# Performance work log

Measured on AMD Instinct MI355X. Metric: run time of the kernel, lower is better.

The kernel has to match this reference:

```python
import jax, jax.numpy as jnp
from jax import lax
import numpy as np

# correlation hyperparams (from init_kwargs)
MAX_D = 32      # maxDisplacement
PAD = 1         # zero padding
K = 3           # patch (kernel) size
STRIDE_K = 1    # stride over output pixels
STRIDE_D = 1    # stride over displacements


def setup_inputs() -> dict:
    key = jax.random.key(0)
    k0, k1 = jax.random.split(key)
    x0 = jax.random.normal(k0, (4, 64, 256, 512), dtype=jnp.float32)
    x1 = jax.random.normal(k1, (4, 64, 256, 512), dtype=jnp.float32)
    return {"x0": x0, "x1": x1}


def _corr2d(x0, x1):
    # x0, x1: [B, C, H, W] NCHW feature maps
    B, C, H, W = x0.shape
    # zero-pad spatially; x1 gets extra width padding so all displacements are in-bounds
    x0p = jnp.pad(x0, ((0, 0), (0, 0), (PAD, PAD), (PAD, PAD)))
    x1p = jnp.pad(x1, ((0, 0), (0, 0), (PAD, PAD), (PAD + MAX_D, PAD + MAX_D)))
    Wp = W + 2 * PAD
    # width offsets into x1p for displacements d = -MAX_D .. MAX_D step STRIDE_D
    offsets = jnp.arange(0, 2 * MAX_D + 1, STRIDE_D, dtype=jnp.int32)

    def step(carry, off):
        x1s = lax.dynamic_slice_in_dim(x1p, off, Wp, axis=3)   # [B,C,Hp,Wp]
        prod = jnp.sum(x0p * x1s, axis=1)                      # channel dot -> [B,Hp,Wp]
        # KxK box-sum over the patch, stride STRIDE_K -> [B,Ho,Wo]
        s = lax.reduce_window(prod, jnp.float32(0), lax.add,
                              (1, K, K), (1, STRIDE_K, STRIDE_K), 'VALID')
        return carry, s

    _, out = lax.scan(step, None, offsets)        # [nD, B, Ho, Wo]
    out = jnp.transpose(out, (1, 0, 2, 3))        # [B, nD, Ho, Wo]
    return out / jnp.asarray(K * K * C, out.dtype)


def reference(x0, x1):
    return _corr2d(x0, x1)
```

## Files before the change

kernel.cpp:

```cpp
#include <hip/hip_runtime.h>

#define WF 512
#define HF 256
#define CF 64
#define NDTOT 65
#define DP 72

static constexpr size_t CH  = (size_t)HF * WF;
static constexpr size_t WH  = (size_t)HF * WF;
static constexpr float  INV = 1.0f / 576.0f;

typedef _Float16 f16;
typedef _Float16 f16x4 __attribute__((ext_vector_type(4)));
typedef _Float16 f16x8 __attribute__((ext_vector_type(8)));
typedef float    f32x4 __attribute__((ext_vector_type(4)));

#if __has_builtin(__builtin_amdgcn_mfma_f32_16x16x16f16)
#define MFMA16(A, B, C) __builtin_amdgcn_mfma_f32_16x16x16f16((A), (B), (C), 0, 0, 0)
#define FRAG_T f16x4
__device__ __forceinline__ f16x4 mkfrag(f16 a, f16 b, f16 c, f16 d) {
    f16x4 r; r[0] = a; r[1] = b; r[2] = c; r[3] = d; return r;
}
#else
#define MFMA16(A, B, C) __builtin_amdgcn_mfma_f32_16x16x32_f16((A), (B), (C), 0, 0, 0)
#define FRAG_T f16x8
__device__ __forceinline__ f16x8 mkfrag(f16 a, f16 b, f16 c, f16 d) {
    f16x8 r; r[0] = a; r[1] = b; r[2] = c; r[3] = d;
    r[4] = (f16)0.f; r[5] = (f16)0.f; r[6] = (f16)0.f; r[7] = (f16)0.f; return r;
}
#endif

#define GLOADF(dst, ptr, offbytes) \
    asm volatile("global_load_dword %0, %1, %2" \
                 : "=v"(dst) : "v"(offbytes), "s"(ptr))

__global__ __launch_bounds__(256) __attribute__((amdgpu_waves_per_eu(2, 4)))
void corr_gram(const float* __restrict__ x0, const float* __restrict__ x1,
               f16* __restrict__ ws) {
    const int f = blockIdx.x;
    const int tid = (f & 7) * 512 + (f >> 3);
    const int b = tid >> 10;
    const int y = (tid >> 2) & 255;
    const int sg = tid & 3;

    const int t = threadIdx.x;
    const int l = t & 63;
    const int w = t >> 6;
    const int xs = (sg * 4 + w) * 32;
    const int jb = xs - 32;

    const int n  = l & 15;
    const int kq = l >> 4;
    const int sn = (n & 3) ^ (n >> 2);

    __shared__ float lds[8192];
    float* base = lds + w * 2048;

    const float* x0r = x0 + (size_t)b * CF * CH + (size_t)y * WF;
    const float* x1r = x1 + (size_t)b * CF * CH + (size_t)y * WF;

    const int c0 = l & 31, qa = l >> 5;
    const int sA = (c0 & 3) ^ ((c0 >> 2) & 3);
    int aoff[2], awad[2];
    aoff[0] = (4 * qa) * (int)CH + xs + c0;
    aoff[1] = (4 * (qa + 2)) * (int)CH + xs + c0;
    awad[0] = c0 * 16 + 4 * (qa ^ sA);
    awad[1] = c0 * 16 + 4 * ((qa + 2) ^ sA);
    int boff[6], bwad[6];
#pragma unroll
    for (int u = 0; u < 6; ++u) {
        const int v = u * 64 + l;
        const int q = v / 96;
        const int cb = v - 96 * q;
        int jg = jb + cb;
        jg = jg < 0 ? 0 : (jg > 511 ? 511 : jg);
        boff[u] = (4 * q) * (int)CH + jg;
        bwad[u] = 512 + cb * 16 + 4 * (q ^ ((cb & 3) ^ ((cb >> 2) & 3)));
    }

    int ard[2], brd[6];
#pragma unroll
    for (int xt = 0; xt < 2; ++xt) ard[xt] = (16 * xt + n) * 16 + 4 * (kq ^ sn);
#pragma unroll
    for (int jt = 0; jt < 6; ++jt) brd[jt] = 512 + (16 * jt + n) * 16 + 4 * (kq ^ sn);
    bool okj[6];
#pragma unroll
    for (int jt = 0; jt < 6; ++jt) okj[jt] = (unsigned)(jb + 16 * jt + n) < (unsigned)WF;

    f32x4 acc[10];
#pragma unroll
    for (int i = 0; i < 10; ++i) acc[i] = (f32x4)0.0f;

    float ra[8], rb[24];

#define LOADK(kk) do { \
    const int kb4 = 4 * (16 * (kk) * (int)CH); \
    _Pragma("unroll") for (int j = 0; j < 2; ++j) \
    _Pragma("unroll") for (int i = 0; i < 4; ++i) \
        GLOADF(ra[4*j+i], x0r, 4 * aoff[j] + kb4 + 4 * i * (int)CH); \
    _Pragma("unroll") for (int u = 0; u < 6; ++u) \
    _Pragma("unroll") for (int i = 0; i < 4; ++i) \
        GLOADF(rb[4*u+i], x1r, 4 * boff[u] + kb4 + 4 * i * (int)CH); \
    __builtin_amdgcn_sched_barrier(0); \
} while (0)

#define TRIPLE(ai, AH, AL) do { \
    acc[ai] = MFMA16(AH, bh, acc[ai]); \
    acc[ai] = MFMA16(AH, bl, acc[ai]); \
    acc[ai] = MFMA16(AL, bh, acc[ai]); } while (0)

    LOADK(0);

#pragma unroll 1
    for (int kk = 0; kk < 4; ++kk) {
        asm volatile("s_waitcnt vmcnt(0)" ::: "memory");
        __builtin_amdgcn_sched_barrier(0);

#pragma unroll
        for (int j = 0; j < 2; ++j)
            *(float4*)&base[awad[j]] = make_float4(ra[4*j], ra[4*j+1], ra[4*j+2], ra[4*j+3]);
#pragma unroll
        for (int u = 0; u < 6; ++u)
            *(float4*)&base[bwad[u]] = make_float4(rb[4*u], rb[4*u+1], rb[4*u+2], rb[4*u+3]);

        if (kk < 3) LOADK(kk + 1);

        FRAG_T ah[2], al[2];
#pragma unroll
        for (int xt = 0; xt < 2; ++xt) {
            const float4 fa = *(const float4*)&base[ard[xt]];
            const float tmp[4] = {fa.x, fa.y, fa.z, fa.w};
            f16 h0 = (f16)tmp[0], h1 = (f16)tmp[1], h2 = (f16)tmp[2], h3 = (f16)tmp[3];
            ah[xt] = mkfrag(h0, h1, h2, h3);
            al[xt] = mkfrag((f16)(tmp[0] - (float)h0), (f16)(tmp[1] - (float)h1),
                            (f16)(tmp[2] - (float)h2), (f16)(tmp[3] - (float)h3));
        }
#pragma unroll
        for (int jt = 0; jt < 6; ++jt) {
            const float4 fb = *(const float4*)&base[brd[jt]];
            float tmp[4] = {fb.x, fb.y, fb.z, fb.w};
#pragma unroll
            for (int i = 0; i < 4; ++i) tmp[i] = okj[jt] ? tmp[i] : 0.f;
            f16 h0 = (f16)tmp[0], h1 = (f16)tmp[1], h2 = (f16)tmp[2], h3 = (f16)tmp[3];
            const FRAG_T bh = mkfrag(h0, h1, h2, h3);
            const FRAG_T bl = mkfrag((f16)(tmp[0] - (float)h0), (f16)(tmp[1] - (float)h1),
                                     (f16)(tmp[2] - (float)h2), (f16)(tmp[3] - (float)h3));
            if (jt < 5)  TRIPLE(jt, ah[0], al[0]);
            if (jt >= 1) TRIPLE(4 + jt, ah[1], al[1]);
        }
    }
#undef TRIPLE
#undef LOADK

    f16* eb = (f16*)base;
#pragma unroll
    for (int xt = 0; xt < 2; ++xt) {
#pragma unroll
        for (int p = 0; p < 5; ++p) {
            const int i = xt * 5 + p;
#pragma unroll
            for (int q = 0; q < 4; ++q) {
                const int m = kq * 4 + q;
                const int xl = xt * 16 + m;
                const int d = 16 * p + n - m;
                if ((unsigned)d < (unsigned)NDTOT)
                    eb[xl * DP + d] = (f16)acc[i][q];
            }
        }
    }
#pragma unroll
    for (int i = 0; i < 4; ++i) {
        const int idx = l + 64 * i;
        if (idx < 224) {
            const int xl = idx / 7;
            eb[xl * DP + NDTOT + (idx - 7 * xl)] = (f16)0.f;
        }
    }
    uint4* dst = (uint4*)(ws + ((size_t)(b * HF + y) * WF + xs) * DP);
    const uint4* src = (const uint4*)eb;
#pragma unroll
    for (int i = 0; i < 5; ++i) {
        const int idx = l + 64 * i;
        if (idx < 288) dst[idx] = src[idx];
    }
}

__global__ __launch_bounds__(256)
void corr_box(const f16* __restrict__ ws, float* __restrict__ out) {
    const int xt = blockIdx.x;
    const int yt = blockIdx.y;
    const int b = blockIdx.z;
    const int t = threadIdx.x;
    const int x0b = xt * 32, y0 = yt * 8;

    __shared__ f16 S[10 * 34][DP];

    for (int u = 0; u < 10; ++u) {
        const int yy = y0 - 1 + u;
        const bool yok = (unsigned)yy < (unsigned)HF;
        const f16* src = ws + ((size_t)(b * HF + yy) * WF + (x0b - 1)) * DP;
#pragma unroll
        for (int sub = 0; sub < 2; ++sub) {
            const int idx = sub * 256 + t;
            if (idx < 306) {
                const int v = idx / 9, dg = idx - v * 9;
                const int xx = x0b - 1 + v;
                f16x8 val;
#pragma unroll
                for (int jj = 0; jj < 8; ++jj) val[jj] = (f16)0.f;
                if (yok && (unsigned)xx < (unsigned)WF)
                    val = *(const f16x8*)(src + (size_t)v * DP + dg * 8);
                *(f16x8*)&S[u * 34 + v][dg * 8] = val;
            }
        }
    }
    __syncthreads();

    const int ly = t >> 5, lx = t & 31;
    const int yg = y0 + ly, xg = x0b + lx;
    float* o0 = out + (size_t)b * NDTOT * WH + (size_t)yg * WF + xg;

#pragma unroll 1
    for (int dg = 0; dg < 9; ++dg) {
        f16x8 s;
#pragma unroll
        for (int jj = 0; jj < 8; ++jj) s[jj] = (f16)0.f;
#pragma unroll
        for (int du = 0; du < 3; ++du)
#pragma unroll
            for (int dv = 0; dv < 3; ++dv)
                s += *(const f16x8*)&S[(ly + du) * 34 + (lx + dv)][dg * 8];
#pragma unroll
        for (int jj = 0; jj < 8; ++jj) {
            const int d = dg * 8 + jj;
            if (d < NDTOT) o0[(size_t)d * WH] = (float)s[jj] * INV;
        }
    }
}

__global__ void corr_naive(const float* __restrict__ x0, const float* __restrict__ x1,
                           float* __restrict__ out) {
    const size_t total = (size_t)4 * NDTOT * WH;
    size_t idx = (size_t)blockIdx.x * blockDim.x + threadIdx.x;
    if (idx >= total) return;
    const int j = (int)(idx % WF);
    const int i = (int)((idx / WF) % HF);
    const int d = (int)((idx / WH) % NDTOT);
    const int b = (int)(idx / ((size_t)NDTOT * WH));
    const int disp = d - 32;
    float s = 0.f;
    for (int u = i - 1; u <= i + 1; ++u) {
        if (u < 0 || u >= HF) continue;
        for (int v = j - 1; v <= j + 1; ++v) {
            if (v < 0 || v >= WF) continue;
            const int v1c = v + disp;
            if (v1c < 0 || v1c >= WF) continue;
            const float* p0 = x0 + (size_t)b * CF * CH + (size_t)u * WF + v;
            const float* p1 = x1 + (size_t)b * CF * CH + (size_t)u * WF + v1c;
            for (int c = 0; c < CF; ++c)
                s += p0[(size_t)c * CH] * p1[(size_t)c * CH];
        }
    }
    out[idx] = s * INV;
}

extern "C" void kernel_launch(void* const* d_in, const int* in_sizes, int n_in,
                              void* d_out, int out_size, void* d_ws, size_t ws_size,
                              hipStream_t stream) {
    const float* x0 = (const float*)d_in[0];
    const float* x1 = (const float*)d_in[1];
    float* out = (float*)d_out;

    const size_t wsNeed = (size_t)4 * HF * WF * DP * sizeof(f16);

    if (ws_size >= wsNeed) {
        f16* ws = (f16*)d_ws;
        corr_gram<<<dim3(4096), dim3(256), 0, stream>>>(x0, x1, ws);
        corr_box<<<dim3(16, 32, 4), dim3(256), 0, stream>>>(ws, out);
    } else {
        const size_t total = (size_t)4 * NDTOT * WH;
        const int blocks = (int)((total + 255) / 256);
        corr_naive<<<dim3(blocks), dim3(256), 0, stream>>>(x0, x1, out);
    }
}
```

Before: 128.0 us.

## Load MFMA fragments directly from global memory with double-buffered registers

```diff
diff --git a/kernel.cpp b/kernel.cpp
--- a/kernel.cpp
+++ b/kernel.cpp
@@ -51,56 +51,38 @@
 
     const int n  = l & 15;
     const int kq = l >> 4;
-    const int sn = (n & 3) ^ (n >> 2);
-
-    __shared__ float lds[8192];
-    float* base = lds + w * 2048;
+
+    __shared__ f16 ebs[4][2304];
 
     const float* x0r = x0 + (size_t)b * CF * CH + (size_t)y * WF;
     const float* x1r = x1 + (size_t)b * CF * CH + (size_t)y * WF;
 
-    const int c0 = l & 31, qa = l >> 5;
-    const int sA = (c0 & 3) ^ ((c0 >> 2) & 3);
-    int aoff[2], awad[2];
-    aoff[0] = (4 * qa) * (int)CH + xs + c0;
-    aoff[1] = (4 * (qa + 2)) * (int)CH + xs + c0;
-    awad[0] = c0 * 16 + 4 * (qa ^ sA);
-    awad[1] = c0 * 16 + 4 * ((qa + 2) ^ sA);
-    int boff[6], bwad[6];
-#pragma unroll
-    for (int u = 0; u < 6; ++u) {
-        const int v = u * 64 + l;
-        const int q = v / 96;
-        const int cb = v - 96 * q;
-        int jg = jb + cb;
-        jg = jg < 0 ? 0 : (jg > 511 ? 511 : jg);
-        boff[u] = (4 * q) * (int)CH + jg;
-        bwad[u] = 512 + cb * 16 + 4 * (q ^ ((cb & 3) ^ ((cb >> 2) & 3)));
-    }
-
-    int ard[2], brd[6];
-#pragma unroll
-    for (int xt = 0; xt < 2; ++xt) ard[xt] = (16 * xt + n) * 16 + 4 * (kq ^ sn);
-#pragma unroll
-    for (int jt = 0; jt < 6; ++jt) brd[jt] = 512 + (16 * jt + n) * 16 + 4 * (kq ^ sn);
-    bool okj[6];
-#pragma unroll
-    for (int jt = 0; jt < 6; ++jt) okj[jt] = (unsigned)(jb + 16 * jt + n) < (unsigned)WF;
+    int aB[2];
+#pragma unroll
+    for (int xt = 0; xt < 2; ++xt)
+        aB[xt] = (4 * kq * (int)CH + xs + 16 * xt + n) * 4;
+    int bB[6]; bool okj[6];
+#pragma unroll
+    for (int jt = 0; jt < 6; ++jt) {
+        int col = jb + 16 * jt + n;
+        okj[jt] = (unsigned)col < (unsigned)WF;
+        col = col < 0 ? 0 : (col > 511 ? 511 : col);
+        bB[jt] = (4 * kq * (int)CH + col) * 4;
+    }
 
     f32x4 acc[10];
 #pragma unroll
     for (int i = 0; i < 10; ++i) acc[i] = (f32x4)0.0f;
 
-    float ra[8], rb[24];
-
-#define LOADK(kk) do { \
-    const int kb4 = 4 * (16 * (kk) * (int)CH); \
-    _Pragma("unroll") for (int j = 0; j < 2; ++j) \
+    float raA[8], rbA[24], raB[8], rbB[24];
+
+#define ISSUE(kk, RA, RB) do { \
+    _Pragma("unroll") for (int xt = 0; xt < 2; ++xt) \
     _Pragma("unroll") for (int i = 0; i < 4; ++i) \
-        GLOADF(ra[4*j+i], x0r, 4 * aoff[j] + kb4 + 4 * i * (int)CH); \
-    _Pragma("unroll") for (int u = 0; u < 6; ++u) \
+        GLOADF(RA[4*xt+i], x0r, aB[xt] + (16*(kk)+i) * (int)(CH*4)); \
+    _Pragma("unroll") for (int jt = 0; jt < 6; ++jt) \
     _Pragma("unroll") for (int i = 0; i < 4; ++i) \
-        GLOADF(rb[4*u+i], x1r, 4 * boff[u] + kb4 + 4 * i * (int)CH); \
+        GLOADF(RB[4*jt+i], x1r, bB[jt] + (16*(kk)+i) * (int)(CH*4)); \
     __builtin_amdgcn_sched_barrier(0); \
 } while (0)
 
@@ -109,50 +91,54 @@
     acc[ai] = MFMA16(AH, bl, acc[ai]); \
     acc[ai] = MFMA16(AL, bh, acc[ai]); } while (0)
 
-    LOADK(0);
-
-#pragma unroll 1
-    for (int kk = 0; kk < 4; ++kk) {
-        asm volatile("s_waitcnt vmcnt(0)" ::: "memory");
-        __builtin_amdgcn_sched_barrier(0);
-
-#pragma unroll
-        for (int j = 0; j < 2; ++j)
-            *(float4*)&base[awad[j]] = make_float4(ra[4*j], ra[4*j+1], ra[4*j+2], ra[4*j+3]);
-#pragma unroll
-        for (int u = 0; u < 6; ++u)
-            *(float4*)&base[bwad[u]] = make_float4(rb[4*u], rb[4*u+1], rb[4*u+2], rb[4*u+3]);
-
-        if (kk < 3) LOADK(kk + 1);
-
-        FRAG_T ah[2], al[2];
-#pragma unroll
-        for (int xt = 0; xt < 2; ++xt) {
-            const float4 fa = *(const float4*)&base[ard[xt]];
-            const float tmp[4] = {fa.x, fa.y, fa.z, fa.w};
-            f16 h0 = (f16)tmp[0], h1 = (f16)tmp[1], h2 = (f16)tmp[2], h3 = (f16)tmp[3];
-            ah[xt] = mkfrag(h0, h1, h2, h3);
-            al[xt] = mkfrag((f16)(tmp[0] - (float)h0), (f16)(tmp[1] - (float)h1),
-                            (f16)(tmp[2] - (float)h2), (f16)(tmp[3] - (float)h3));
-        }
-#pragma unroll
-        for (int jt = 0; jt < 6; ++jt) {
-            const float4 fb = *(const float4*)&base[brd[jt]];
-            float tmp[4] = {fb.x, fb.y, fb.z, fb.w};
-#pragma unroll
-            for (int i = 0; i < 4; ++i) tmp[i] = okj[jt] ? tmp[i] : 0.f;
-            f16 h0 = (f16)tmp[0], h1 = (f16)tmp[1], h2 = (f16)tmp[2], h3 = (f16)tmp[3];
-            const FRAG_T bh = mkfrag(h0, h1, h2, h3);
-            const FRAG_T bl = mkfrag((f16)(tmp[0] - (float)h0), (f16)(tmp[1] - (float)h1),
-                                     (f16)(tmp[2] - (float)h2), (f16)(tmp[3] - (float)h3));
-            if (jt < 5)  TRIPLE(jt, ah[0], al[0]);
-            if (jt >= 1) TRIPLE(4 + jt, ah[1], al[1]);
-        }
-    }
+#define COMPUTE(RA, RB) do { \
+    FRAG_T ah[2], al[2]; \
+    _Pragma("unroll") for (int xt = 0; xt < 2; ++xt) { \
+        const float v0 = RA[4*xt], v1 = RA[4*xt+1], v2 = RA[4*xt+2], v3 = RA[4*xt+3]; \
+        const f16 h0 = (f16)v0, h1 = (f16)v1, h2 = (f16)v2, h3 = (f16)v3; \
+        ah[xt] = mkfrag(h0, h1, h2, h3); \
+        al[xt] = mkfrag((f16)(v0 - (float)h0), (f16)(v1 - (float)h1), \
+                        (f16)(v2 - (float)h2), (f16)(v3 - (float)h3)); \
+    } \
+    _Pragma("unroll") for (int jt = 0; jt < 6; ++jt) { \
+        float v0 = RB[4*jt], v1 = RB[4*jt+1], v2 = RB[4*jt+2], v3 = RB[4*jt+3]; \
+        v0 = okj[jt] ? v0 : 0.f; v1 = okj[jt] ? v1 : 0.f; \
+        v2 = okj[jt] ? v2 : 0.f; v3 = okj[jt] ? v3 : 0.f; \
+        const f16 h0 = (f16)v0, h1 = (f16)v1, h2 = (f16)v2, h3 = (f16)v3; \
+        const FRAG_T bh = mkfrag(h0, h1, h2, h3); \
+        const FRAG_T bl = mkfrag((f16)(v0 - (float)h0), (f16)(v1 - (float)h1), \
+                                 (f16)(v2 - (float)h2), (f16)(v3 - (float)h3)); \
+        if (jt < 5)  TRIPLE(jt, ah[0], al[0]); \
+        if (jt >= 1) TRIPLE(4 + jt, ah[1], al[1]); \
+    } \
+} while (0)
+
+#define WAIT32() do { asm volatile("s_waitcnt vmcnt(32)" ::: "memory"); \
+                      __builtin_amdgcn_sched_barrier(0); } while (0)
+#define WAIT0()  do { asm volatile("s_waitcnt vmcnt(0)" ::: "memory"); \
+                      __builtin_amdgcn_sched_barrier(0); } while (0)
+
+    ISSUE(0, raA, rbA);
+    ISSUE(1, raB, rbB);
+
+    WAIT32();
+    COMPUTE(raA, rbA);
+    ISSUE(2, raA, rbA);
+    WAIT32();
+    COMPUTE(raB, rbB);
+    ISSUE(3, raB, rbB);
+    WAIT32();
+    COMPUTE(raA, rbA);
+    WAIT0();
+    COMPUTE(raB, rbB);
+
+#undef COMPUTE
 #undef TRIPLE
-#undef LOADK
-
-    f16* eb = (f16*)base;
+#undef ISSUE
+#undef WAIT32
+#undef WAIT0
+
+    f16* eb = ebs[w];
 #pragma unroll
     for (int xt = 0; xt < 2; ++xt) {
 #pragma unroll
```

Result: slower. 133.1 us (+4.0%).
